# Optimization experiments

Hardware: AMD Instinct MI355X
Metric: run time of the kernel (lower is better)

The kernel has to match this reference:

```python
import jax, jax.numpy as jnp
import numpy as np

D_MODEL = 4096
N_TYPES = 6  # fixed event_types list in the module


def setup_inputs() -> dict:
    key = jax.random.key(0)
    ks = jax.random.split(key, 7)
    E, B, d = 131072, 16384, D_MODEL
    return {
        "event_type": jax.random.randint(ks[0], (E,), 0, N_TYPES),
        "confidence": jax.random.uniform(ks[1], (E,), jnp.float32),
        "location": jax.random.uniform(ks[2], (E, 2), jnp.float32) * jnp.array([640.0, 480.0], jnp.float32),
        "batch_idx": jax.random.randint(ks[3], (E,), 0, B),
        "batch_size": B,
        "type_emb": jax.random.normal(ks[4], (N_TYPES, d // 4), jnp.float32),
        "W1": jax.random.normal(ks[5], (d // 2, d // 4 + 3), jnp.float32) / np.sqrt(d // 4 + 3).astype(np.float32),
        "b1": jnp.zeros((d // 2,), jnp.float32),
        "W2": jax.random.normal(ks[6], (d, d // 2), jnp.float32) / np.sqrt(d // 2).astype(np.float32),
        "b2": jnp.zeros((d,), jnp.float32),
    }


def reference(event_type, confidence, location, batch_idx, batch_size, type_emb, W1, b1, W2, b2):
    E = confidence.shape[0]
    B = batch_size
    # per-batch-slot max confidence (empty slots -> -inf)
    seg_max = jax.ops.segment_max(confidence, batch_idx, num_segments=B)
    is_top = confidence == seg_max[batch_idx]
    # first event attaining the max (matches torch's max-over-list semantics)
    cand = jnp.where(is_top, jnp.arange(E), E)
    top_idx = jnp.full((B,), E, dtype=cand.dtype).at[batch_idx].min(cand)
    has_event = top_idx < E
    safe_idx = jnp.where(has_event, top_idx, 0)

    emb = type_emb[event_type[safe_idx]]                 # [B, d/4]
    c = confidence[safe_idx][:, None]                    # [B, 1]
    loc = location[safe_idx] / jnp.array([640.0, 480.0], jnp.float32)  # [B, 2]
    feats = jnp.concatenate([emb, c, loc], axis=-1)      # [B, d/4 + 3]

    h = jax.nn.relu(feats @ W1.T + b1)                   # [B, d/2]
    out = h @ W2.T + b2                                  # [B, d]
    return jnp.where(has_event[:, None], out, jnp.zeros((), out.dtype))
```

## Files before the change

kernel.cpp:

```cpp
#include <hip/hip_runtime.h>
#include <hip/hip_bf16.h>

#define NT 6
#define BM 256
#define BN 256
#define BK 64
#define SLOT_S 32768
#define AH1 8192
#define BH0 16384
#define BH1 24576

typedef __attribute__((ext_vector_type(4))) float f32x4;
typedef __attribute__((ext_vector_type(8))) short bf16x8;

__device__ __forceinline__ short f2bf(float f) {
    __hip_bfloat16 h = __float2bfloat16(f);
    return (short)__builtin_bit_cast(unsigned short, h);
}

__global__ void k_segmax(const float* __restrict__ conf,
                         const int* __restrict__ bidx,
                         unsigned long long* __restrict__ packed, int E) {
    int i = blockIdx.x * blockDim.x + threadIdx.x;
    if (i >= E) return;
    unsigned cb = __float_as_uint(conf[i]);
    unsigned long long p = ((unsigned long long)cb << 32) | (unsigned)(~(unsigned)i);
    atomicMax(&packed[bidx[i]], p);
}

__global__ void k_base(const float* __restrict__ emb, const float* __restrict__ W1,
                       const float* __restrict__ b1, float* __restrict__ base,
                       float* __restrict__ vecs, int d2, int d4) {
    int gw = (blockIdx.x * blockDim.x + threadIdx.x) >> 6;
    int lane = threadIdx.x & 63;
    int t = gw / d2, n = gw % d2;
    const float* e = emb + (size_t)t * d4;
    const float* w = W1 + (size_t)n * (d4 + 3);
    float s = 0.f;
    for (int k = lane; k < d4; k += 64) s += e[k] * w[k];
#pragma unroll
    for (int m = 32; m; m >>= 1) s += __shfl_xor(s, m);
    if (lane == 0) {
        base[gw] = s + b1[n];
        if (t == 0) {
            vecs[n]          = w[d4];
            vecs[d2 + n]     = w[d4 + 1];
            vecs[2 * d2 + n] = w[d4 + 2];
        }
    }
}

__global__ void k_w2cast(const float* __restrict__ W2, short* __restrict__ W2b, long n) {
    long i = ((long)blockIdx.x * blockDim.x + threadIdx.x) * 8;
    if (i >= n) return;
    bf16x8 v;
#pragma unroll
    for (int j = 0; j < 8; ++j) v[j] = f2bf(W2[i + j]);
    *(bf16x8*)(W2b + i) = v;
}

__global__ void k_h(const unsigned long long* __restrict__ packed,
                    const int* __restrict__ etype, const float* __restrict__ loc,
                    const float* __restrict__ base, const float* __restrict__ vecs,
                    float* __restrict__ mask, short* __restrict__ h, int d2) {
    int b = blockIdx.x;
    int tid = threadIdx.x;
    unsigned long long p = packed[b];
    bool has = (p != 0ULL);
    float conf = 0.f, lx = 0.f, ly = 0.f;
    int t = 0;
    if (has) {
        unsigned idx = ~(unsigned)(p & 0xFFFFFFFFu);
        conf = __uint_as_float((unsigned)(p >> 32));
        t  = etype[idx];
        lx = loc[2 * (size_t)idx]     * (1.0f / 640.0f);
        ly = loc[2 * (size_t)idx + 1] * (1.0f / 480.0f);
    }
    if (tid == 0) mask[b] = has ? 1.0f : 0.0f;
    const float* bs = base + (size_t)t * d2;
    const float* cv = vecs;
    const float* xv = vecs + d2;
    const float* yv = vecs + 2 * d2;
    int n0 = tid * 8;
    bf16x8 v;
#pragma unroll
    for (int j = 0; j < 8; ++j) {
        int n = n0 + j;
        float g = bs[n] + conf * cv[n] + lx * xv[n] + ly * yv[n];
        g = fmaxf(g, 0.f);
        v[j] = has ? f2bf(g) : (short)0;
    }
    *(bf16x8*)(h + (size_t)b * d2 + n0) = v;
}


#define GLL(src, dst) __builtin_amdgcn_global_load_lds(                      \
    (const __attribute__((address_space(1))) void*)(src),                    \
    (__attribute__((address_space(3))) void*)(dst), 16, 0, 0)

#define SB __builtin_amdgcn_sched_barrier(0)

#define ST_AH0(ws, kt) { GLL(pA + (size_t)(kt) * 64, (ws) + dst1);           \
                         GLL(pA + (size_t)64 * K + (kt) * 64, (ws) + dst2); }
#define ST_AH1(ws, kt) { GLL(pA + (size_t)128 * K + (kt) * 64, (ws) + AH1 + dst1); \
                         GLL(pA + (size_t)192 * K + (kt) * 64, (ws) + AH1 + dst2); }
#define ST_BH0(ws, kt) { GLL(pB + (size_t)(kt) * 64, (ws) + BH0 + dst1);     \
                         GLL(pB + (size_t)64 * K + (kt) * 64, (ws) + BH0 + dst2); }
#define ST_BH1(ws, kt) { GLL(pB + (size_t)128 * K + (kt) * 64, (ws) + BH1 + dst1); \
                         GLL(pB + (size_t)192 * K + (kt) * 64, (ws) + BH1 + dst2); }

#define MFMA16(AI, NI, BVV)                                                  \
    _Pragma("unroll") for (int m = 0; m < 4; ++m)                            \
    _Pragma("unroll") for (int n = 0; n < 2; ++n) {                          \
        acc[(AI) + m][(NI) + n] = __builtin_amdgcn_mfma_f32_16x16x32_bf16(   \
            aA[m][0], BVV[n][0], acc[(AI) + m][(NI) + n], 0, 0, 0);          \
        acc[(AI) + m][(NI) + n] = __builtin_amdgcn_mfma_f32_16x16x32_bf16(   \
            aA[m][1], BVV[n][1], acc[(AI) + m][(NI) + n], 0, 0, 0);          \
    }

__global__ __launch_bounds__(512, 2)
void k_gemm(const short* __restrict__ A, const short* __restrict__ Bm,
            const float* __restrict__ b2, const float* __restrict__ mask,
            float* __restrict__ C, int M, int N, int K, int nbn) {
    __shared__ __align__(16) short lds[2 * SLOT_S];

    int tid = threadIdx.x;
    int lane = tid & 63;
    int wave = tid >> 6;
    int wr = wave >> 2, wc = wave & 3;

    int bid = blockIdx.x;
    int wg = (bid & 7) * ((int)gridDim.x >> 3) + (bid >> 3);
    int bm = wg / nbn, bn = wg % nbn;
    int row0 = bm * BM, col0 = bn * BN;

    int r1 = tid >> 3;
    int pg = tid & 7;
    int cg = pg ^ (r1 & 7);
    const short* pA = A + (size_t)(row0 + r1) * K + cg * 8;
    const short* pB = Bm + (size_t)(col0 + r1) * K + cg * 8;
    int dst1 = tid * 8;
    int dst2 = 4096 + tid * 8;

    int frow = lane & 15, fk = lane >> 4;
    int kx = frow & 7;
    int aoffs0 = (wr * 64 + frow) * 64 + ((fk) ^ kx) * 8;
    int aoffs1 = (wr * 64 + frow) * 64 + ((4 + fk) ^ kx) * 8;
    int boffs0 = (wc * 32 + frow) * 64 + ((fk) ^ kx) * 8;
    int boffs1 = (wc * 32 + frow) * 64 + ((4 + fk) ^ kx) * 8;

    f32x4 acc[8][4] = {};
    bf16x8 aA[4][2], bB0[2][2], bB1[2][2];

    int KT = K / BK;

    ST_AH0(lds, 0); ST_BH0(lds, 0); ST_BH1(lds, 0); ST_AH1(lds, 0);
    asm volatile("s_waitcnt vmcnt(0)" ::: "memory");
    __builtin_amdgcn_s_barrier();
    SB;

#pragma unroll 1
    for (int t = 0; t < KT; ++t) {
        const short* sl = lds + (t & 1) * SLOT_S;
        short* wsl = lds + ((t + 1) & 1) * SLOT_S;
        bool stg = (t < KT - 1);

#pragma unroll
        for (int n = 0; n < 2; ++n) {
            bB0[n][0] = *(const bf16x8*)(sl + BH0 + boffs0 + n * 1024);
            bB0[n][1] = *(const bf16x8*)(sl + BH0 + boffs1 + n * 1024);
        }
#pragma unroll
        for (int m = 0; m < 4; ++m) {
            aA[m][0] = *(const bf16x8*)(sl + aoffs0 + m * 1024);
            aA[m][1] = *(const bf16x8*)(sl + aoffs1 + m * 1024);
        }
        if (stg) { ST_AH0(wsl, t + 1); ST_BH0(wsl, t + 1); }
        SB;
        __builtin_amdgcn_s_barrier();
        asm volatile("s_waitcnt lgkmcnt(0)" ::: "memory");
        SB;
        __builtin_amdgcn_s_setprio(1);
        MFMA16(0, 0, bB0)
        __builtin_amdgcn_s_setprio(0);
        SB;
        if (stg) asm volatile("s_waitcnt vmcnt(6)" ::: "memory");
        else     asm volatile("s_waitcnt vmcnt(2)" ::: "memory");
        __builtin_amdgcn_s_barrier();

#pragma unroll
        for (int n = 0; n < 2; ++n) {
            bB1[n][0] = *(const bf16x8*)(sl + BH1 + boffs0 + n * 1024);
            bB1[n][1] = *(const bf16x8*)(sl + BH1 + boffs1 + n * 1024);
        }
        if (stg) ST_BH1(wsl, t + 1);
        SB;
        __builtin_amdgcn_s_barrier();
        asm volatile("s_waitcnt lgkmcnt(0)" ::: "memory");
        SB;
        __builtin_amdgcn_s_setprio(1);
        MFMA16(0, 2, bB1)
        __builtin_amdgcn_s_setprio(0);
        SB;
        if (stg) asm volatile("s_waitcnt vmcnt(6)" ::: "memory");
        else     asm volatile("s_waitcnt vmcnt(0)" ::: "memory");
        __builtin_amdgcn_s_barrier();

#pragma unroll
        for (int m = 0; m < 4; ++m) {
            aA[m][0] = *(const bf16x8*)(sl + AH1 + aoffs0 + m * 1024);
            aA[m][1] = *(const bf16x8*)(sl + AH1 + aoffs1 + m * 1024);
        }
        if (stg) ST_AH1(wsl, t + 1);
        SB;
        __builtin_amdgcn_s_barrier();
        asm volatile("s_waitcnt lgkmcnt(0)" ::: "memory");
        SB;
        __builtin_amdgcn_s_setprio(1);
        MFMA16(4, 2, bB1)
        __builtin_amdgcn_s_setprio(0);
        SB;

        __builtin_amdgcn_s_setprio(1);
        MFMA16(4, 0, bB0)
        __builtin_amdgcn_s_setprio(0);
        SB;
        if (stg) {
            asm volatile("s_waitcnt vmcnt(4)" ::: "memory");
            __builtin_amdgcn_s_barrier();
            SB;
        }
    }

#pragma unroll
    for (int mi = 0; mi < 8; ++mi) {
        int rbase = row0 + (mi >> 2) * 128 + wr * 64 + (mi & 3) * 16 + fk * 4;
#pragma unroll
        for (int j = 0; j < 4; ++j) {
            int r = rbase + j;
            float mk = mask[r];
#pragma unroll
            for (int ni = 0; ni < 4; ++ni) {
                int cc = col0 + (ni >> 1) * 128 + wc * 32 + (ni & 1) * 16 + frow;
                C[(size_t)r * N + cc] = (acc[mi][ni][j] + b2[cc]) * mk;
            }
        }
    }
}

extern "C" void kernel_launch(void* const* d_in, const int* in_sizes, int n_in,
                              void* d_out, int out_size, void* d_ws, size_t ws_size,
                              hipStream_t stream) {
    const int* etype   = (const int*)d_in[0];
    const float* conf  = (const float*)d_in[1];
    const float* loc   = (const float*)d_in[2];
    const int* bidx    = (const int*)d_in[3];
    const float* emb   = (const float*)d_in[5];
    const float* W1    = (const float*)d_in[6];
    const float* b1    = (const float*)d_in[7];
    const float* W2    = (const float*)d_in[8];
    const float* b2    = (const float*)d_in[9];
    float* out = (float*)d_out;

    int E  = in_sizes[0];
    int d2 = in_sizes[7];
    int d  = in_sizes[9];
    int d4 = in_sizes[5] / NT;
    int B  = out_size / d;

    char* ws = (char*)d_ws;
    unsigned long long* packed = (unsigned long long*)ws;
    float* mask = (float*)(ws + (size_t)B * 8);
    float* base = mask + B;
    float* vecs = base + NT * d2;
    short* w2b  = (short*)(vecs + 3 * d2);
    short* h    = w2b + (size_t)d * d2;

    hipMemsetAsync(packed, 0, (size_t)B * 8, stream);
    k_segmax<<<(E + 255) / 256, 256, 0, stream>>>(conf, bidx, packed, E);
    k_base<<<(NT * d2) / 4, 256, 0, stream>>>(emb, W1, b1, base, vecs, d2, d4);
    long nw2 = (long)d * d2;
    k_w2cast<<<(int)(nw2 / 8 / 256), 256, 0, stream>>>(W2, w2b, nw2);
    k_h<<<B, 256, 0, stream>>>(packed, etype, loc, base, vecs, mask, h, d2);
    int nbm = B / BM, nbn = d / BN;
    k_gemm<<<dim3(nbm * nbn), dim3(512), 0, stream>>>(h, w2b, b2, mask, out, B, d, d2, nbn);
}
```

Measured before the change: 307.4 us.

## Replace four-phase interleaved GEMM pipeline with single load-then-compute stage per tile

Removes the hand-scheduled four-phase K-loop, which staged A and B halves in separate steps with sched_barriers, partial vmcnt waits and several barriers per tile. Each tile now reads all A and B fragments from LDS at once, issues every global-to-LDS prefetch for the next tile, runs all 64 MFMAs, and then waits on vmcnt(0) plus one barrier. This cuts barriers and wait instructions and lets the compiler schedule freely. In exchange it loses the fine-grained overlap of LDS reads with MFMA work and raises fragment register pressure.

```diff
diff --git a/kernel.cpp b/kernel.cpp
--- a/kernel.cpp
+++ b/kernel.cpp
@@ -98,8 +98,6 @@
     (const __attribute__((address_space(1))) void*)(src),                    \
     (__attribute__((address_space(3))) void*)(dst), 16, 0, 0)
 
-#define SB __builtin_amdgcn_sched_barrier(0)
-
 #define ST_AH0(ws, kt) { GLL(pA + (size_t)(kt) * 64, (ws) + dst1);           \
                          GLL(pA + (size_t)64 * K + (kt) * 64, (ws) + dst2); }
 #define ST_AH1(ws, kt) { GLL(pA + (size_t)128 * K + (kt) * 64, (ws) + AH1 + dst1); \
@@ -109,15 +107,6 @@
 #define ST_BH1(ws, kt) { GLL(pB + (size_t)128 * K + (kt) * 64, (ws) + BH1 + dst1); \
                          GLL(pB + (size_t)192 * K + (kt) * 64, (ws) + BH1 + dst2); }
 
-#define MFMA16(AI, NI, BVV)                                                  \
-    _Pragma("unroll") for (int m = 0; m < 4; ++m)                            \
-    _Pragma("unroll") for (int n = 0; n < 2; ++n) {                          \
-        acc[(AI) + m][(NI) + n] = __builtin_amdgcn_mfma_f32_16x16x32_bf16(   \
-            aA[m][0], BVV[n][0], acc[(AI) + m][(NI) + n], 0, 0, 0);          \
-        acc[(AI) + m][(NI) + n] = __builtin_amdgcn_mfma_f32_16x16x32_bf16(   \
-            aA[m][1], BVV[n][1], acc[(AI) + m][(NI) + n], 0, 0, 0);          \
-    }
-
 __global__ __launch_bounds__(512, 2)
 void k_gemm(const short* __restrict__ A, const short* __restrict__ Bm,
             const float* __restrict__ b2, const float* __restrict__ mask,
@@ -150,85 +139,57 @@
     int boffs1 = (wc * 32 + frow) * 64 + ((4 + fk) ^ kx) * 8;
 
     f32x4 acc[8][4] = {};
-    bf16x8 aA[4][2], bB0[2][2], bB1[2][2];
+    bf16x8 aA[8][2], bB[4][2];
 
     int KT = K / BK;
 
     ST_AH0(lds, 0); ST_BH0(lds, 0); ST_BH1(lds, 0); ST_AH1(lds, 0);
     asm volatile("s_waitcnt vmcnt(0)" ::: "memory");
     __builtin_amdgcn_s_barrier();
-    SB;
 
 #pragma unroll 1
     for (int t = 0; t < KT; ++t) {
         const short* sl = lds + (t & 1) * SLOT_S;
         short* wsl = lds + ((t + 1) & 1) * SLOT_S;
-        bool stg = (t < KT - 1);
-
+
+#pragma unroll
+        for (int m = 0; m < 4; ++m) {
+            aA[m][0]     = *(const bf16x8*)(sl + aoffs0 + m * 1024);
+            aA[m][1]     = *(const bf16x8*)(sl + aoffs1 + m * 1024);
+        }
 #pragma unroll
         for (int n = 0; n < 2; ++n) {
-            bB0[n][0] = *(const bf16x8*)(sl + BH0 + boffs0 + n * 1024);
-            bB0[n][1] = *(const bf16x8*)(sl + BH0 + boffs1 + n * 1024);
+            bB[n][0]     = *(const bf16x8*)(sl + BH0 + boffs0 + n * 1024);
+            bB[n][1]     = *(const bf16x8*)(sl + BH0 + boffs1 + n * 1024);
+            bB[2 + n][0] = *(const bf16x8*)(sl + BH1 + boffs0 + n * 1024);
+            bB[2 + n][1] = *(const bf16x8*)(sl + BH1 + boffs1 + n * 1024);
         }
 #pragma unroll
         for (int m = 0; m < 4; ++m) {
-            aA[m][0] = *(const bf16x8*)(sl + aoffs0 + m * 1024);
-            aA[m][1] = *(const bf16x8*)(sl + aoffs1 + m * 1024);
-        }
-        if (stg) { ST_AH0(wsl, t + 1); ST_BH0(wsl, t + 1); }
-        SB;
-        __builtin_amdgcn_s_barrier();
-        asm volatile("s_waitcnt lgkmcnt(0)" ::: "memory");
-        SB;
+            aA[4 + m][0] = *(const bf16x8*)(sl + AH1 + aoffs0 + m * 1024);
+            aA[4 + m][1] = *(const bf16x8*)(sl + AH1 + aoffs1 + m * 1024);
+        }
+
+        if (t < KT - 1) {
+            ST_AH0(wsl, t + 1); ST_BH0(wsl, t + 1);
+            ST_BH1(wsl, t + 1); ST_AH1(wsl, t + 1);
+        }
+
         __builtin_amdgcn_s_setprio(1);
-        MFMA16(0, 0, bB0)
+#pragma unroll
+        for (int m = 0; m < 8; ++m)
+#pragma unroll
+            for (int n = 0; n < 4; ++n) {
+                acc[m][n] = __builtin_amdgcn_mfma_f32_16x16x32_bf16(
+                    aA[m][0], bB[n][0], acc[m][n], 0, 0, 0);
+                acc[m][n] = __builtin_amdgcn_mfma_f32_16x16x32_bf16(
+                    aA[m][1], bB[n][1], acc[m][n], 0, 0, 0);
+            }
         __builtin_amdgcn_s_setprio(0);
-        SB;
-        if (stg) asm volatile("s_waitcnt vmcnt(6)" ::: "memory");
-        else     asm volatile("s_waitcnt vmcnt(2)" ::: "memory");
-        __builtin_amdgcn_s_barrier();
-
-#pragma unroll
-        for (int n = 0; n < 2; ++n) {
-            bB1[n][0] = *(const bf16x8*)(sl + BH1 + boffs0 + n * 1024);
-            bB1[n][1] = *(const bf16x8*)(sl + BH1 + boffs1 + n * 1024);
-        }
-        if (stg) ST_BH1(wsl, t + 1);
-        SB;
-        __builtin_amdgcn_s_barrier();
-        asm volatile("s_waitcnt lgkmcnt(0)" ::: "memory");
-        SB;
-        __builtin_amdgcn_s_setprio(1);
-        MFMA16(0, 2, bB1)
-        __builtin_amdgcn_s_setprio(0);
-        SB;
-        if (stg) asm volatile("s_waitcnt vmcnt(6)" ::: "memory");
-        else     asm volatile("s_waitcnt vmcnt(0)" ::: "memory");
-        __builtin_amdgcn_s_barrier();
-
-#pragma unroll
-        for (int m = 0; m < 4; ++m) {
-            aA[m][0] = *(const bf16x8*)(sl + AH1 + aoffs0 + m * 1024);
-            aA[m][1] = *(const bf16x8*)(sl + AH1 + aoffs1 + m * 1024);
-        }
-        if (stg) ST_AH1(wsl, t + 1);
-        SB;
-        __builtin_amdgcn_s_barrier();
-        asm volatile("s_waitcnt lgkmcnt(0)" ::: "memory");
-        SB;
-        __builtin_amdgcn_s_setprio(1);
-        MFMA16(4, 2, bB1)
-        __builtin_amdgcn_s_setprio(0);
-        SB;
-
-        __builtin_amdgcn_s_setprio(1);
-        MFMA16(4, 0, bB0)
-        __builtin_amdgcn_s_setprio(0);
-        SB;
-        if (stg) {
-            asm volatile("s_waitcnt vmcnt(4)" ::: "memory");
+
+        if (t < KT - 1) {
+            asm volatile("s_waitcnt vmcnt(0)" ::: "memory");
             __builtin_amdgcn_s_barrier();
-            SB;
         }
     }
 
```

New measurement: 295.6 us. 3.9% less time.
